# Kernel tuning notes

Measured on AMD Instinct MI355X. Metric: run time of the kernel, lower is better.

Reference implementation:

```python
import jax, jax.numpy as jnp
import numpy as np

EMBED = 960
NUM_CLASSES = 10
LN_EPS = 1e-5


def _linear_params(key, fan_in, fan_out):
    kw, kb = jax.random.split(key)
    bound = 1.0 / np.sqrt(fan_in)
    W = jax.random.uniform(kw, (fan_out, fan_in), jnp.float32, -bound, bound)
    b = jax.random.uniform(kb, (fan_out,), jnp.float32, -bound, bound)
    return W, b


def setup_inputs() -> dict:
    key = jax.random.key(0)
    ks = jax.random.split(key, 10)
    B, S, D = 32, 1024, EMBED
    x = jax.random.normal(ks[0], (B, S, D), jnp.float32)
    mask = jax.random.randint(ks[1], (B, S), 0, 2, jnp.int32)
    Wq, bq = _linear_params(ks[2], D, D)
    Wk, bk = _linear_params(ks[3], D, D)
    Wv, bv = _linear_params(ks[4], D, D)
    ln_g = jnp.ones((D,), jnp.float32)
    ln_b = jnp.zeros((D,), jnp.float32)
    W1, b1 = _linear_params(ks[5], D, 512)
    W2, b2 = _linear_params(ks[6], 512, 256)
    W3, b3 = _linear_params(ks[7], 256, 128)
    W4, b4 = _linear_params(ks[8], 128, NUM_CLASSES)
    return dict(x=x, mask=mask, Wq=Wq, bq=bq, Wk=Wk, bk=bk, Wv=Wv, bv=bv,
                ln_g=ln_g, ln_b=ln_b, W1=W1, b1=b1, W2=W2, b2=b2,
                W3=W3, b3=b3, W4=W4, b4=b4)


def reference(x, mask, Wq, bq, Wk, bk, Wv, bv, ln_g, ln_b,
              W1, b1, W2, b2, W3, b3, W4, b4):
    D = x.shape[-1]
    # single-head self-attention (hand-rolled, full NxN scores)
    Q = jnp.einsum('bsd,ed->bse', x, Wq) + bq
    K = jnp.einsum('bsd,ed->bse', x, Wk) + bk
    V = jnp.einsum('bsd,ed->bse', x, Wv) + bv
    scores = jnp.einsum('bqd,bkd->bqk', Q, K) / np.sqrt(D)  # [B,S,S]
    scores = jnp.where(mask[:, None, :] == 0, -1e9, scores)
    attn = jax.nn.softmax(scores, axis=-1)
    context = jnp.einsum('bqk,bkd->bqd', attn, V)
    # residual + LayerNorm
    h = context + x
    mu = jnp.mean(h, axis=-1, keepdims=True)
    var = jnp.mean(jnp.square(h - mu), axis=-1, keepdims=True)
    ctx = (h - mu) * jax.lax.rsqrt(var + LN_EPS) * ln_g + ln_b
    # masked mean pool
    mf = mask[:, :, None].astype(jnp.float32)  # [B,S,1]
    pooled = (ctx * mf).sum(axis=1) / jnp.clip(mf.sum(axis=1), 1e-9)
    # MLP (dropout inactive in eval mode)
    h = jax.nn.relu(pooled @ W1.T + b1)
    h = jax.nn.relu(h @ W2.T + b2)
    h = jax.nn.relu(h @ W3.T + b3)
    return h @ W4.T + b4
```

## Files before the change

kernel.cpp:

```cpp
#include <hip/hip_runtime.h>


#define DEVINL __device__ __forceinline__

typedef __attribute__((ext_vector_type(8))) short bf16x8;
typedef __attribute__((ext_vector_type(4))) float f32x4;
typedef __attribute__((ext_vector_type(4))) unsigned short u16x4;

DEVINL unsigned short f2bf(float f) {
  unsigned int u = __float_as_uint(f);
  u += 0x7FFFu + ((u >> 16) & 1u);
  return (unsigned short)(u >> 16);
}

DEVINL float bf2f(unsigned short h) { return __uint_as_float(((unsigned int)h) << 16); }

DEVINL void gload_lds16(const void* g, void* l) {
  __builtin_amdgcn_global_load_lds((const __attribute__((address_space(1))) unsigned int*)g,
                                   (__attribute__((address_space(3))) unsigned int*)l,
                                   16, 0, 0);
}

#define MFMA16(a, b, c) __builtin_amdgcn_mfma_f32_16x16x32_bf16((a), (b), (c), 0, 0, 0)

__global__ __launch_bounds__(256) void scan_mask(
    const int* __restrict__ mask, int* __restrict__ idx, int* __restrict__ cnt) {
  __shared__ int ps[256];
  const int b = blockIdx.x, t = threadIdx.x;
  const int4 m = *(const int4*)(mask + b * 1024 + t * 4);
  const int s = (m.x != 0) + (m.y != 0) + (m.z != 0) + (m.w != 0);
  ps[t] = s;
  __syncthreads();
  for (int off = 1; off < 256; off <<= 1) {
    const int v = (t >= off) ? ps[t - off] : 0;
    __syncthreads();
    ps[t] += v;
    __syncthreads();
  }
  int pos = ps[t] - s;
  if (m.x) idx[b * 1024 + pos++] = t * 4 + 0;
  if (m.y) idx[b * 1024 + pos++] = t * 4 + 1;
  if (m.z) idx[b * 1024 + pos++] = t * 4 + 2;
  if (m.w) idx[b * 1024 + pos++] = t * 4 + 3;
  if (t == 255) cnt[b] = ps[255];
}

__global__ __launch_bounds__(256) void cast_wqkv(
    const float* __restrict__ Wq, const float* __restrict__ Wk, const float* __restrict__ Wv,
    const float* __restrict__ bq, const float* __restrict__ bk, const float* __restrict__ bv,
    unsigned short* __restrict__ Wqkv, float* __restrict__ biasQ, float scaleQ) {
  const int r = blockIdx.x, t = threadIdx.x;
  const int seg = (r >= 1920) ? 2 : (r >= 960 ? 1 : 0);
  const int sr = r - seg * 960;
  const float* W = (seg == 0) ? Wq : (seg == 1) ? Wk : Wv;
  const float sc = (seg == 0) ? scaleQ : 1.0f;
  if (t < 240) {
    f32x4 v = *(const f32x4*)(W + (size_t)sr * 960 + t * 4);
    u16x4 o;
    o[0] = f2bf(v[0] * sc); o[1] = f2bf(v[1] * sc);
    o[2] = f2bf(v[2] * sc); o[3] = f2bf(v[3] * sc);
    *(u16x4*)(Wqkv + (size_t)r * 1024 + t * 4) = o;
  } else {
    u16x4 z = {};
    *(u16x4*)(Wqkv + (size_t)r * 1024 + 960 + (t - 240) * 4) = z;
  }
  if (t == 0) {
    const float* bb = (seg == 0) ? bq : (seg == 1) ? bk : bv;
    biasQ[r] = bb[sr] * sc;
  }
}

__global__ __launch_bounds__(256) void compact_x(
    const float* __restrict__ x, const int* __restrict__ idx, const int* __restrict__ cnt,
    unsigned short* __restrict__ xc) {
  const int b = blockIdx.y;
  const int j = blockIdx.x * 4 + (threadIdx.x >> 6);
  const int l = threadIdx.x & 63;
  const int cb = cnt[b];
  const int cbc = (cb + 127) & ~127;
  if (j >= cbc) return;
  unsigned short* o = xc + ((size_t)b * 1024 + j) * 1024 + l * 16;
  bf16x8 o0 = {}, o1 = {};
  if (j < cb && l < 60) {
    const int s = idx[b * 1024 + j];
    const float* g = x + ((size_t)b * 1024 + s) * 960 + l * 16;
    f32x4 v0 = *(const f32x4*)(g);
    f32x4 v1 = *(const f32x4*)(g + 4);
    f32x4 v2 = *(const f32x4*)(g + 8);
    f32x4 v3 = *(const f32x4*)(g + 12);
    o0[0] = (short)f2bf(v0[0]); o0[1] = (short)f2bf(v0[1]);
    o0[2] = (short)f2bf(v0[2]); o0[3] = (short)f2bf(v0[3]);
    o0[4] = (short)f2bf(v1[0]); o0[5] = (short)f2bf(v1[1]);
    o0[6] = (short)f2bf(v1[2]); o0[7] = (short)f2bf(v1[3]);
    o1[0] = (short)f2bf(v2[0]); o1[1] = (short)f2bf(v2[1]);
    o1[2] = (short)f2bf(v2[2]); o1[3] = (short)f2bf(v2[3]);
    o1[4] = (short)f2bf(v3[0]); o1[5] = (short)f2bf(v3[1]);
    o1[6] = (short)f2bf(v3[2]); o1[7] = (short)f2bf(v3[3]);
  }
  *(bf16x8*)(o) = o0;
  *(bf16x8*)(o + 8) = o1;
}

template <int MODE>
__global__ __launch_bounds__(256, 2) void gemm128(
    const unsigned short* __restrict__ Ap, const unsigned short* __restrict__ Bp,
    int lda, int ldb, const float* __restrict__ bias,
    unsigned short* __restrict__ outC, unsigned short* __restrict__ outQ,
    unsigned short* __restrict__ outK, unsigned short* __restrict__ outV,
    int mTiles, int nTiles, int nktFixed, int ncols, int ldo,
    size_t aStride, size_t bStride, size_t oStride, const int* __restrict__ cntArr) {
  __shared__ unsigned short As[2][128 * 64];
  __shared__ unsigned short Bs[2][128 * 64];
  const int t = threadIdx.x, l = t & 63, w = t >> 6;
  const int wr = w >> 1, wc = w & 1;
  const int lq = l & 15, lh = l >> 4;

  const int nwg = (int)gridDim.x;
  const int flat = (int)blockIdx.x;
  const int q8 = nwg >> 3, r8 = nwg & 7, xcd = flat & 7;
  const int wgid = (xcd < r8 ? xcd * (q8 + 1) : r8 * (q8 + 1) + (xcd - r8) * q8) + (flat >> 3);
  const int pt = mTiles * nTiles;
  const int zb = wgid / pt;
  const int rm = wgid - zb * pt;
  const int mi = rm / nTiles;
  const int m0 = mi * 128;
  const int n0 = (rm - mi * nTiles) * 128;

  const int cb = cntArr[zb];
  if (m0 >= cb) return;
  const int nkt = (MODE == 2) ? ((cb + 63) >> 6) : nktFixed;

  const unsigned short* A = Ap + (size_t)zb * aStride + (size_t)m0 * lda;
  const unsigned short* B = Bp + (size_t)zb * bStride + (size_t)n0 * ldb;

#define STAGEG(D0, BB)                                                        \
  {                                                                           \
    _Pragma("unroll") for (int q_ = 0; q_ < 4; ++q_) {                        \
      const int r_ = q_ * 32 + w * 8 + (l >> 3);                              \
      const int sg_ = (l & 7) ^ (r_ & 7);                                     \
      gload_lds16(A + (size_t)r_ * lda + (D0) + sg_ * 8,                      \
                  (char*)&As[BB][(size_t)(q_ * 32 + w * 8) * 64]);            \
      gload_lds16(B + (size_t)r_ * ldb + (D0) + sg_ * 8,                      \
                  (char*)&Bs[BB][(size_t)(q_ * 32 + w * 8) * 64]);            \
    }                                                                         \
  }

  f32x4 acc[4][4] = {};
  STAGEG(0, 0);
  int buf = 0;
  for (int kt = 0; kt < nkt; ++kt) {
    if (kt + 1 < nkt) {
      STAGEG((kt + 1) * 64, buf ^ 1);
      asm volatile("s_waitcnt vmcnt(8)" ::: "memory");
    } else {
      asm volatile("s_waitcnt vmcnt(0)" ::: "memory");
    }
    __builtin_amdgcn_sched_barrier(0);
    __builtin_amdgcn_s_barrier();
    bf16x8 aF[2][4], bF[2][4];
#pragma unroll
    for (int h = 0; h < 2; ++h)
#pragma unroll
      for (int i = 0; i < 4; ++i) {
        const int rowA = 64 * wr + 16 * i + lq;
        aF[h][i] = *(const bf16x8*)&As[buf][(size_t)rowA * 64 +
                                           (size_t)(((h << 2) | lh) ^ (rowA & 7)) * 8];
        const int rowB = 64 * wc + 16 * i + lq;
        bF[h][i] = *(const bf16x8*)&Bs[buf][(size_t)rowB * 64 +
                                           (size_t)(((h << 2) | lh) ^ (rowB & 7)) * 8];
      }
#pragma unroll
    for (int h = 0; h < 2; ++h)
#pragma unroll
      for (int i = 0; i < 4; ++i)
#pragma unroll
        for (int j = 0; j < 4; ++j) acc[i][j] = MFMA16(aF[h][i], bF[h][j], acc[i][j]);
    __builtin_amdgcn_s_barrier();
    buf ^= 1;
  }
#undef STAGEG

  if (MODE == 2) {
#pragma unroll
    for (int j = 0; j < 4; ++j) {
      const int col = n0 + 64 * wc + 16 * j + lq;
      if (col >= ncols) continue;
#pragma unroll
      for (int i = 0; i < 4; ++i)
#pragma unroll
        for (int r = 0; r < 4; ++r) {
          const int row = m0 + 64 * wr + 16 * i + 4 * lh + r;
          outC[(size_t)zb * oStride + (size_t)row * ldo + col] = f2bf(acc[i][j][r]);
        }
    }
  } else {
#pragma unroll
    for (int j = 0; j < 4; ++j) {
      const int col = n0 + 64 * wc + 16 * j + lq;
      if (col >= ncols) continue;
      const int seg = (col >= 1920) ? 2 : (col >= 960 ? 1 : 0);
      const int dcol = col - seg * 960;
      const float bv = bias[col];
#pragma unroll
      for (int i = 0; i < 4; ++i)
#pragma unroll
        for (int r = 0; r < 4; ++r) {
          const int row = m0 + 64 * wr + 16 * i + 4 * lh + r;
          const unsigned short v = f2bf(acc[i][j][r] + bv);
          if (seg == 0) outQ[((size_t)zb * 1024 + row) * 960 + dcol] = v;
          else if (seg == 1) outK[((size_t)zb * 1024 + row) * 960 + dcol] = v;
          else outV[((size_t)zb << 20) + ((size_t)dcol << 10) + row] = v;
        }
    }
  }
}

__global__ __launch_bounds__(512, 2) void attn_softmax(
    const unsigned short* __restrict__ Qb, const unsigned short* __restrict__ Kb,
    const int* __restrict__ cnt, unsigned short* __restrict__ P) {
  __shared__ unsigned short Ks[2][1024 * 32];
  __shared__ unsigned short Qs[2][64 * 32];
  __shared__ float red[2][8][64];
  const int t = threadIdx.x, l = t & 63, w = t >> 6;
  const int flat = blockIdx.x;
  const int b = (flat & 7) * 4 + ((flat >> 3) >> 4);
  const int q0 = ((flat >> 3) & 15) * 64;
  const int cb = cnt[b];
  if (q0 >= cb) return;
  const int nks = (cb + 127) >> 7;
  const int lq = l & 15, lh = l >> 4;
  const size_t kbase = (size_t)b * 1024 * 960;
  const size_t qbase = ((size_t)b * 1024 + q0) * 960;
  const int lr = l >> 2, sg0 = l & 3;

#define STAGE(kkv, bufv)                                                      \
  {                                                                           \
    const int d0_ = (kkv) * 32;                                               \
    _Pragma("unroll") for (int i_ = 0; i_ < 8; ++i_) {                        \
      const int br_ = i_ * 128 + w * 16;                                      \
      const int kr_ = (i_ < nks) ? (br_ + lr) : (w * 16 + lr);                \
      const int sg_ = sg0 ^ ((kr_ >> 1) & 3);                                 \
      gload_lds16(Kb + kbase + (size_t)kr_ * 960 + d0_ + sg_ * 8,             \
                  (char*)Ks[(bufv)] + (size_t)br_ * 64);                      \
    }                                                                         \
    {                                                                         \
      const int qw_ = w & 3;                                                  \
      const int qr_ = qw_ * 16 + lr;                                          \
      const int sg_ = sg0 ^ ((qr_ >> 1) & 3);                                 \
      gload_lds16(Qb + qbase + (size_t)qr_ * 960 + d0_ + sg_ * 8,             \
                  (char*)Qs[(bufv)] + (size_t)(qw_ * 16) * 64);               \
    }                                                                         \
  }

  f32x4 acc[4][8] = {};
  STAGE(0, 0);
  int buf = 0;
  for (int kk = 0; kk < 30; ++kk) {
    if (kk < 29) {
      STAGE(kk + 1, buf ^ 1);
      asm volatile("s_waitcnt vmcnt(9)" ::: "memory");
    } else {
      asm volatile("s_waitcnt vmcnt(0)" ::: "memory");
    }
    __builtin_amdgcn_sched_barrier(0);
    __builtin_amdgcn_s_barrier();
    if (w < nks) {
      bf16x8 aF[4], bF[8];
#pragma unroll
      for (int i = 0; i < 4; ++i) {
        const int qr = 16 * i + lq;
        aF[i] = *(const bf16x8*)(Qs[buf] + qr * 32 + (lh ^ ((qr >> 1) & 3)) * 8);
      }
#pragma unroll
      for (int j = 0; j < 8; ++j) {
        const int kr = 128 * w + 16 * j + lq;
        bF[j] = *(const bf16x8*)(Ks[buf] + kr * 32 + (lh ^ ((kr >> 1) & 3)) * 8);
      }
#pragma unroll
      for (int i = 0; i < 4; ++i)
#pragma unroll
        for (int j = 0; j < 8; ++j) acc[i][j] = MFMA16(aF[i], bF[j], acc[i][j]);
    }
    __builtin_amdgcn_s_barrier();
    buf ^= 1;
  }
#undef STAGE

#pragma unroll
  for (int j = 0; j < 8; ++j) {
    const int k = 128 * w + 16 * j + lq;
    if (k >= cb) {
#pragma unroll
      for (int i = 0; i < 4; ++i)
#pragma unroll
        for (int r = 0; r < 4; ++r) acc[i][j][r] = -1e9f;
    }
  }

  float rmax[4][4];
#pragma unroll
  for (int i = 0; i < 4; ++i)
#pragma unroll
    for (int r = 0; r < 4; ++r) {
      float m = acc[i][0][r];
#pragma unroll
      for (int j = 1; j < 8; ++j) m = fmaxf(m, acc[i][j][r]);
      m = fmaxf(m, __shfl_xor(m, 1));
      m = fmaxf(m, __shfl_xor(m, 2));
      m = fmaxf(m, __shfl_xor(m, 4));
      m = fmaxf(m, __shfl_xor(m, 8));
      rmax[i][r] = m;
    }
  if (lq == 0) {
#pragma unroll
    for (int i = 0; i < 4; ++i)
#pragma unroll
      for (int r = 0; r < 4; ++r) red[0][w][16 * i + 4 * lh + r] = rmax[i][r];
  }
  __syncthreads();
#pragma unroll
  for (int i = 0; i < 4; ++i)
#pragma unroll
    for (int r = 0; r < 4; ++r) {
      const int rowi = 16 * i + 4 * lh + r;
      float m = red[0][0][rowi];
#pragma unroll
      for (int w2 = 1; w2 < 8; ++w2) m = fmaxf(m, red[0][w2][rowi]);
      rmax[i][r] = m;
    }

  float rsum[4][4];
#pragma unroll
  for (int i = 0; i < 4; ++i)
#pragma unroll
    for (int r = 0; r < 4; ++r) {
      float s = 0.f;
#pragma unroll
      for (int j = 0; j < 8; ++j) {
        const float e = __expf(acc[i][j][r] - rmax[i][r]);
        acc[i][j][r] = e;
        s += e;
      }
      s += __shfl_xor(s, 1); s += __shfl_xor(s, 2);
      s += __shfl_xor(s, 4); s += __shfl_xor(s, 8);
      rsum[i][r] = s;
    }
  if (lq == 0) {
#pragma unroll
    for (int i = 0; i < 4; ++i)
#pragma unroll
      for (int r = 0; r < 4; ++r) red[1][w][16 * i + 4 * lh + r] = rsum[i][r];
  }
  __syncthreads();

  if (w < nks) {
    const size_t pb = ((size_t)b << 20) + (size_t)q0 * 1024;
#pragma unroll
    for (int i = 0; i < 4; ++i)
#pragma unroll
      for (int r = 0; r < 4; ++r) {
        const int rowi = 16 * i + 4 * lh + r;
        float s = 0.f;
#pragma unroll
        for (int w2 = 0; w2 < 8; ++w2) s += red[1][w2][rowi];
        const float inv = 1.0f / s;
#pragma unroll
        for (int j = 0; j < 8; ++j) {
          const int col = 128 * w + 16 * j + lq;
          P[pb + (size_t)rowi * 1024 + col] = f2bf(acc[i][j][r] * inv);
        }
      }
  }
}

__global__ __launch_bounds__(256) void ln_pool(
    const unsigned short* __restrict__ ctxb, const float* __restrict__ x,
    const int* __restrict__ idx, const int* __restrict__ cnt,
    const float* __restrict__ g, const float* __restrict__ bta,
    float* __restrict__ pooled) {
  const int b = blockIdx.y, chunk = blockIdx.x;
  const int w = threadIdx.x >> 6, l = threadIdx.x & 63;
  const int cb = cnt[b];
  f32x4 gc[4], bc[4];
#pragma unroll
  for (int c = 0; c < 4; ++c) {
    const int i4 = c * 64 + l;
    if (i4 < 240) {
      gc[c] = *(const f32x4*)(g + i4 * 4);
      bc[c] = *(const f32x4*)(bta + i4 * 4);
    }
  }
  f32x4 accp[4] = {};
  for (int rr = 0; rr < 8; ++rr) {
    const int j = chunk * 32 + w * 8 + rr;
    if (j >= cb) continue;
    const int sidx = idx[b * 1024 + j];
    const size_t cbase = ((size_t)b * 1024 + j) * 960;
    const size_t xbase = ((size_t)b * 1024 + sidx) * 960;
    f32x4 h[4];
    float part = 0.f;
#pragma unroll
    for (int c = 0; c < 4; ++c) {
      const int i4 = c * 64 + l;
      if (i4 < 240) {
        u16x4 cv = *(const u16x4*)(ctxb + cbase + (size_t)i4 * 4);
        f32x4 xv = *(const f32x4*)(x + xbase + (size_t)i4 * 4);
        h[c][0] = bf2f(cv[0]) + xv[0];
        h[c][1] = bf2f(cv[1]) + xv[1];
        h[c][2] = bf2f(cv[2]) + xv[2];
        h[c][3] = bf2f(cv[3]) + xv[3];
        part += h[c][0] + h[c][1] + h[c][2] + h[c][3];
      } else {
        h[c] = 0;
      }
    }
#pragma unroll
    for (int o = 1; o < 64; o <<= 1) part += __shfl_xor(part, o);
    const float mu = part * (1.0f / 960.0f);
    float p2 = 0.f;
#pragma unroll
    for (int c = 0; c < 4; ++c) {
      if (c * 64 + l < 240) {
#pragma unroll
        for (int k2 = 0; k2 < 4; ++k2) {
          const float d = h[c][k2] - mu;
          p2 += d * d;
        }
      }
    }
#pragma unroll
    for (int o = 1; o < 64; o <<= 1) p2 += __shfl_xor(p2, o);
    const float rs = rsqrtf(p2 * (1.0f / 960.0f) + 1e-5f);
#pragma unroll
    for (int c = 0; c < 4; ++c) {
      if (c * 64 + l < 240) {
#pragma unroll
        for (int k2 = 0; k2 < 4; ++k2)
          accp[c][k2] += (h[c][k2] - mu) * rs * gc[c][k2] + bc[c][k2];
      }
    }
  }
#pragma unroll
  for (int c = 0; c < 4; ++c) {
    const int i4 = c * 64 + l;
    if (i4 < 240) {
#pragma unroll
      for (int k2 = 0; k2 < 4; ++k2) atomicAdd(&pooled[b * 960 + i4 * 4 + k2], accp[c][k2]);
    }
  }
}

__global__ __launch_bounds__(256) void mlp_head(
    const float* __restrict__ pooled, const int* __restrict__ cnt,
    const float* __restrict__ W1, const float* __restrict__ b1,
    const float* __restrict__ W2, const float* __restrict__ b2,
    const float* __restrict__ W3, const float* __restrict__ b3,
    const float* __restrict__ W4, const float* __restrict__ b4, float* __restrict__ out) {
  __shared__ float h0[960], h1[512], h2[256], h3[128];
  const int b = blockIdx.x, t = threadIdx.x;
  const float inv = 1.0f / fmaxf((float)cnt[b], 1e-9f);
  for (int d = t; d < 960; d += 256) h0[d] = pooled[b * 960 + d] * inv;
  __syncthreads();
  for (int o = t; o < 512; o += 256) {
    float a = b1[o];
    const float* wr = W1 + (size_t)o * 960;
    for (int k = 0; k < 960; k += 4) {
      f32x4 wv = *(const f32x4*)(wr + k);
      f32x4 hv = *(const f32x4*)(h0 + k);
      a += wv[0] * hv[0] + wv[1] * hv[1] + wv[2] * hv[2] + wv[3] * hv[3];
    }
    h1[o] = fmaxf(a, 0.f);
  }
  __syncthreads();
  {
    float a = b2[t];
    const float* wr = W2 + (size_t)t * 512;
    for (int k = 0; k < 512; k += 4) {
      f32x4 wv = *(const f32x4*)(wr + k);
      f32x4 hv = *(const f32x4*)(h1 + k);
      a += wv[0] * hv[0] + wv[1] * hv[1] + wv[2] * hv[2] + wv[3] * hv[3];
    }
    h2[t] = fmaxf(a, 0.f);
  }
  __syncthreads();
  if (t < 128) {
    float a = b3[t];
    const float* wr = W3 + (size_t)t * 256;
    for (int k = 0; k < 256; k += 4) {
      f32x4 wv = *(const f32x4*)(wr + k);
      f32x4 hv = *(const f32x4*)(h2 + k);
      a += wv[0] * hv[0] + wv[1] * hv[1] + wv[2] * hv[2] + wv[3] * hv[3];
    }
    h3[t] = fmaxf(a, 0.f);
  }
  __syncthreads();
  if (t < 10) {
    float a = b4[t];
    const float* wr = W4 + (size_t)t * 128;
    for (int k = 0; k < 128; ++k) a += wr[k] * h3[k];
    out[b * 10 + t] = a;
  }
}

extern "C" void kernel_launch(void* const* d_in, const int* in_sizes, int n_in,
                              void* d_out, int out_size, void* d_ws, size_t ws_size,
                              hipStream_t stream) {
  (void)in_sizes; (void)n_in; (void)out_size; (void)ws_size;
  const float* x    = (const float*)d_in[0];
  const int*   mask = (const int*)d_in[1];
  const float* Wq   = (const float*)d_in[2];
  const float* bq   = (const float*)d_in[3];
  const float* Wk   = (const float*)d_in[4];
  const float* bk   = (const float*)d_in[5];
  const float* Wv   = (const float*)d_in[6];
  const float* bv   = (const float*)d_in[7];
  const float* lng  = (const float*)d_in[8];
  const float* lnb  = (const float*)d_in[9];
  const float* W1   = (const float*)d_in[10];
  const float* b1   = (const float*)d_in[11];
  const float* W2   = (const float*)d_in[12];
  const float* b2   = (const float*)d_in[13];
  const float* W3   = (const float*)d_in[14];
  const float* b3   = (const float*)d_in[15];
  const float* W4   = (const float*)d_in[16];
  const float* b4   = (const float*)d_in[17];
  float* out = (float*)d_out;

  char* ws = (char*)d_ws;
  unsigned short* xc     = (unsigned short*)(ws);
  unsigned short* P      = (unsigned short*)(ws);
  unsigned short* Qb     = (unsigned short*)(ws + 67108864);
  unsigned short* Kb     = (unsigned short*)(ws + 130023424);
  unsigned short* ctxb   = (unsigned short*)(ws + 67108864);
  unsigned short* Vt     = (unsigned short*)(ws + 192937984);
  unsigned short* Wqkv   = (unsigned short*)(ws + 260046848);
  float*          biasQ  = (float*)(ws + 266338304);
  float*          pooled = (float*)(ws + 266349824);
  int*            cntW   = (int*)(ws + 266472704);
  int*            idxW   = (int*)(ws + 266472832);

  const float scaleQ = 0.0322748612183951f;

  scan_mask<<<32, 256, 0, stream>>>(mask, idxW, cntW);
  cast_wqkv<<<2880, 256, 0, stream>>>(Wq, Wk, Wv, bq, bk, bv, Wqkv, biasQ, scaleQ);
  compact_x<<<dim3(256, 32), 256, 0, stream>>>(x, idxW, cntW, xc);

  gemm128<1><<<32 * 8 * 23, 256, 0, stream>>>(
      xc, Wqkv, 1024, 1024, biasQ, nullptr, Qb, Kb, Vt,
      8, 23, 15, 2880, 0, (size_t)1048576, 0, 0, cntW);

  attn_softmax<<<512, 512, 0, stream>>>(Qb, Kb, cntW, P);

  gemm128<2><<<8 * 8 * 32, 256, 0, stream>>>(
      P, Vt, 1024, 1024, nullptr, ctxb, nullptr, nullptr, nullptr,
      8, 8, 0, 960, 960, (size_t)1048576, (size_t)1048576, (size_t)983040, cntW);

  hipMemsetAsync(pooled, 0, 32 * 960 * 4, stream);
  ln_pool<<<dim3(32, 32), 256, 0, stream>>>(ctxb, x, idxW, cntW, lng, lnb, pooled);
  mlp_head<<<32, 256, 0, stream>>>(pooled, cntW, W1, b1, W2, b2, W3, b3, W4, b4, out);
}
```

Measured before the change: 514.5 us.

## Switch GEMM to single-buffered 32-wide K tiles for higher occupancy

Replaces the double-buffered 64-wide K pipeline in the tiled bf16 GEMM with a single-buffered 32-wide K tile guarded by two __syncthreads per step. This cuts LDS per block to a quarter and raises the launch-bounds occupancy target from 2 to 4 blocks per CU, relying on more resident waves to hide global-load latency. In exchange it drops the prefetch overlap, doubles the number of K iterations and barriers, and uses a new XOR swizzle suited to the narrower rows.

```diff
diff --git a/kernel.cpp b/kernel.cpp
--- a/kernel.cpp
+++ b/kernel.cpp
@@ -102,15 +102,15 @@
 }
 
 template <int MODE>
-__global__ __launch_bounds__(256, 2) void gemm128(
+__global__ __launch_bounds__(256, 4) void gemm128s(
     const unsigned short* __restrict__ Ap, const unsigned short* __restrict__ Bp,
     int lda, int ldb, const float* __restrict__ bias,
     unsigned short* __restrict__ outC, unsigned short* __restrict__ outQ,
     unsigned short* __restrict__ outK, unsigned short* __restrict__ outV,
     int mTiles, int nTiles, int nktFixed, int ncols, int ldo,
     size_t aStride, size_t bStride, size_t oStride, const int* __restrict__ cntArr) {
-  __shared__ unsigned short As[2][128 * 64];
-  __shared__ unsigned short Bs[2][128 * 64];
+  __shared__ unsigned short As[128 * 32];
+  __shared__ unsigned short Bs[128 * 32];
   const int t = threadIdx.x, l = t & 63, w = t >> 6;
   const int wr = w >> 1, wc = w & 1;
   const int lq = l & 15, lh = l >> 4;
@@ -128,57 +128,43 @@
 
   const int cb = cntArr[zb];
   if (m0 >= cb) return;
-  const int nkt = (MODE == 2) ? ((cb + 63) >> 6) : nktFixed;
+  const int nkt = (MODE == 2) ? ((cb + 31) >> 5) : nktFixed;
 
   const unsigned short* A = Ap + (size_t)zb * aStride + (size_t)m0 * lda;
   const unsigned short* B = Bp + (size_t)zb * bStride + (size_t)n0 * ldb;
 
-#define STAGEG(D0, BB)                                                        \
-  {                                                                           \
-    _Pragma("unroll") for (int q_ = 0; q_ < 4; ++q_) {                        \
-      const int r_ = q_ * 32 + w * 8 + (l >> 3);                              \
-      const int sg_ = (l & 7) ^ (r_ & 7);                                     \
-      gload_lds16(A + (size_t)r_ * lda + (D0) + sg_ * 8,                      \
-                  (char*)&As[BB][(size_t)(q_ * 32 + w * 8) * 64]);            \
-      gload_lds16(B + (size_t)r_ * ldb + (D0) + sg_ * 8,                      \
-                  (char*)&Bs[BB][(size_t)(q_ * 32 + w * 8) * 64]);            \
-    }                                                                         \
-  }
+  const int srow0 = w * 16 + (l >> 2);
+  const int sg0 = l & 3;
 
   f32x4 acc[4][4] = {};
-  STAGEG(0, 0);
-  int buf = 0;
   for (int kt = 0; kt < nkt; ++kt) {
-    if (kt + 1 < nkt) {
-      STAGEG((kt + 1) * 64, buf ^ 1);
-      asm volatile("s_waitcnt vmcnt(8)" ::: "memory");
-    } else {
-      asm volatile("s_waitcnt vmcnt(0)" ::: "memory");
-    }
-    __builtin_amdgcn_sched_barrier(0);
-    __builtin_amdgcn_s_barrier();
-    bf16x8 aF[2][4], bF[2][4];
-#pragma unroll
-    for (int h = 0; h < 2; ++h)
-#pragma unroll
-      for (int i = 0; i < 4; ++i) {
-        const int rowA = 64 * wr + 16 * i + lq;
-        aF[h][i] = *(const bf16x8*)&As[buf][(size_t)rowA * 64 +
-                                           (size_t)(((h << 2) | lh) ^ (rowA & 7)) * 8];
-        const int rowB = 64 * wc + 16 * i + lq;
-        bF[h][i] = *(const bf16x8*)&Bs[buf][(size_t)rowB * 64 +
-                                           (size_t)(((h << 2) | lh) ^ (rowB & 7)) * 8];
-      }
-#pragma unroll
-    for (int h = 0; h < 2; ++h)
-#pragma unroll
-      for (int i = 0; i < 4; ++i)
-#pragma unroll
-        for (int j = 0; j < 4; ++j) acc[i][j] = MFMA16(aF[h][i], bF[h][j], acc[i][j]);
-    __builtin_amdgcn_s_barrier();
-    buf ^= 1;
-  }
-#undef STAGEG
+    const int d0 = kt * 32;
+    __syncthreads();
+#pragma unroll
+    for (int p = 0; p < 2; ++p) {
+      const int row = p * 64 + srow0;
+      const int sg = sg0 ^ ((row >> 1) & 3);
+      gload_lds16(A + (size_t)row * lda + d0 + sg * 8,
+                  (char*)As + (size_t)(p * 64 + w * 16) * 64);
+      gload_lds16(B + (size_t)row * ldb + d0 + sg * 8,
+                  (char*)Bs + (size_t)(p * 64 + w * 16) * 64);
+    }
+    __syncthreads();
+    bf16x8 aF[4], bF[4];
+#pragma unroll
+    for (int i = 0; i < 4; ++i) {
+      const int rowA = 64 * wr + 16 * i + lq;
+      aF[i] = *(const bf16x8*)(As + (size_t)rowA * 32 +
+                               (size_t)(lh ^ ((rowA >> 1) & 3)) * 8);
+      const int rowB = 64 * wc + 16 * i + lq;
+      bF[i] = *(const bf16x8*)(Bs + (size_t)rowB * 32 +
+                               (size_t)(lh ^ ((rowB >> 1) & 3)) * 8);
+    }
+#pragma unroll
+    for (int i = 0; i < 4; ++i)
+#pragma unroll
+      for (int j = 0; j < 4; ++j) acc[i][j] = MFMA16(aF[i], bF[j], acc[i][j]);
+  }
 
   if (MODE == 2) {
 #pragma unroll
@@ -545,13 +531,13 @@
   cast_wqkv<<<2880, 256, 0, stream>>>(Wq, Wk, Wv, bq, bk, bv, Wqkv, biasQ, scaleQ);
   compact_x<<<dim3(256, 32), 256, 0, stream>>>(x, idxW, cntW, xc);
 
-  gemm128<1><<<32 * 8 * 23, 256, 0, stream>>>(
+  gemm128s<1><<<32 * 8 * 23, 256, 0, stream>>>(
       xc, Wqkv, 1024, 1024, biasQ, nullptr, Qb, Kb, Vt,
-      8, 23, 15, 2880, 0, (size_t)1048576, 0, 0, cntW);
+      8, 23, 30, 2880, 0, (size_t)1048576, 0, 0, cntW);
 
   attn_softmax<<<512, 512, 0, stream>>>(Qb, Kb, cntW, P);
 
-  gemm128<2><<<8 * 8 * 32, 256, 0, stream>>>(
+  gemm128s<2><<<8 * 8 * 32, 256, 0, stream>>>(
       P, Vt, 1024, 1024, nullptr, ctxb, nullptr, nullptr, nullptr,
       8, 8, 0, 960, 960, (size_t)1048576, (size_t)1048576, (size_t)983040, cntW);
 
```

Result: faster. 503.1 us (-2.2%).
